# Kernel optimization log

Measured on AMD Instinct MI355X. Metric: run time of the kernel, lower is better.

Reference implementation:

```python
import jax, jax.numpy as jnp
import numpy as np

N = 100000
E = 1000000
HID = 64


def gcn_conv(x, W, b, edge_index, edge_w, num_nodes):
    # PyG GCNConv with edge_weight: add self-loops (weight 1), symmetric norm,
    # out[c] = sum_e norm_e * (x @ W)[row_e] aggregated at col_e, plus bias.
    xw = x @ W  # [N, hid]
    row = jnp.concatenate([edge_index[0], jnp.arange(num_nodes)])
    col = jnp.concatenate([edge_index[1], jnp.arange(num_nodes)])
    ew = jnp.concatenate([edge_w, jnp.ones((num_nodes,), x.dtype)])
    deg = jax.ops.segment_sum(ew, col, num_segments=num_nodes)
    dinv = jnp.where(deg > 0, jax.lax.rsqrt(deg), 0.0)
    norm = dinv[row] * ew * dinv[col]  # [E+N]
    msgs = norm[:, None] * xw[row]  # [E+N, hid]
    out = jax.ops.segment_sum(msgs, col, num_segments=num_nodes)
    return out + b


def setup_inputs() -> dict:
    key = jax.random.key(0)
    ks = jax.random.split(key, 12)
    user_x = jax.random.normal(ks[0], (N, 3), jnp.float32)
    movie_x = jax.random.normal(ks[1], (N, 18), jnp.float32)
    edge_index = jax.random.randint(ks[2], (2, E), 0, N, jnp.int64)
    edge_attr = jax.random.uniform(ks[3], (E,), jnp.float32)
    def lin(k, fan_in, fan_out):
        bound = 1.0 / np.sqrt(fan_in)
        k1, k2 = jax.random.split(k)
        W = jax.random.uniform(k1, (fan_in, fan_out), jnp.float32, -bound, bound)
        b = jax.random.uniform(k2, (fan_out,), jnp.float32, -bound, bound)
        return W, b
    W_user, b_user = lin(ks[4], 3, HID)
    W_movie, b_movie = lin(ks[5], 18, HID)
    W1, b1 = lin(ks[6], 2 * HID, 128)
    W2, b2 = lin(ks[7], 128, 1)
    return {"user_x": user_x, "movie_x": movie_x, "edge_index": edge_index,
            "edge_attr": edge_attr, "W_user": W_user, "b_user": b_user,
            "W_movie": W_movie, "b_movie": b_movie, "W1": W1, "b1": b1,
            "W2": W2, "b2": b2}


def reference(user_x, movie_x, edge_index, edge_attr, W_user, b_user,
              W_movie, b_movie, W1, b1, W2, b2):
    user_out = gcn_conv(user_x, W_user, b_user, edge_index, edge_attr, N)
    movie_out = gcn_conv(movie_x, W_movie, b_movie, edge_index, edge_attr, N)
    h = jnp.concatenate([user_out, movie_out], axis=-1)  # [N, 128]
    h = jax.nn.relu(h @ W1 + b1)
    rating_pred = h @ W2 + b2  # [N, 1]
    return rating_pred
```

## Files before the change

### kernel.cpp

```cpp
#include <hip/hip_runtime.h>
#include <hip/hip_fp16.h>

#define NN 100000
#define NE 1000000
#define BSH 7
#define BCOLS 128
#define NBUCK 782
#define SBLK 256
#define SITER 16
#define CAP 2048
#define OVCAP 16384

__device__ __forceinline__ float2 h2f(unsigned u) {
    union { unsigned u; __half2 h; } c; c.u = u;
    return __half22float2(c.h);
}
__device__ __forceinline__ unsigned f2h2(float a, float b) {
    union { __half2 h; unsigned u; } c; c.h = __floats2half2_rn(a, b);
    return c.u;
}

#define ACC_ROW16(base)                                                      \
    {                                                                        \
        const uint4* pr_ = (const uint4*)(base);                             \
        const uint4 A_ = pr_[0];                                             \
        const uint4 B_ = pr_[1];                                             \
        const uint4 C_ = pr_[2];                                             \
        float2 f_;                                                           \
        f_ = h2f(A_.x); s21[0]  = fmaf(w, f_.x, s21[0]);  s21[1]  = fmaf(w, f_.y, s21[1]);  \
        f_ = h2f(A_.y); s21[2]  = fmaf(w, f_.x, s21[2]);  s21[3]  = fmaf(w, f_.y, s21[3]);  \
        f_ = h2f(A_.z); s21[4]  = fmaf(w, f_.x, s21[4]);  s21[5]  = fmaf(w, f_.y, s21[5]);  \
        f_ = h2f(A_.w); s21[6]  = fmaf(w, f_.x, s21[6]);  s21[7]  = fmaf(w, f_.y, s21[7]);  \
        f_ = h2f(B_.x); s21[8]  = fmaf(w, f_.x, s21[8]);  s21[9]  = fmaf(w, f_.y, s21[9]);  \
        f_ = h2f(B_.y); s21[10] = fmaf(w, f_.x, s21[10]); s21[11] = fmaf(w, f_.y, s21[11]); \
        f_ = h2f(B_.z); s21[12] = fmaf(w, f_.x, s21[12]); s21[13] = fmaf(w, f_.y, s21[13]); \
        f_ = h2f(B_.w); s21[14] = fmaf(w, f_.x, s21[14]); s21[15] = fmaf(w, f_.y, s21[15]); \
        f_ = h2f(C_.x); s21[16] = fmaf(w, f_.x, s21[16]); s21[17] = fmaf(w, f_.y, s21[17]); \
        f_ = h2f(C_.y); s21[18] = fmaf(w, f_.x, s21[18]); s21[19] = fmaf(w, f_.y, s21[19]); \
        f_ = h2f(C_.z); s21[20] = fmaf(w, f_.x, s21[20]);                    \
    }

__global__ __launch_bounds__(128) void fuse_kernel(const float* __restrict__ Wu,
                                                   const float* __restrict__ bu,
                                                   const float* __restrict__ Wm,
                                                   const float* __restrict__ bm,
                                                   const float* __restrict__ W1,
                                                   const float* __restrict__ b1,
                                                   const float* __restrict__ W2,
                                                   float* __restrict__ Mt,
                                                   int* __restrict__ gcur,
                                                   int* __restrict__ ovfn) {
    const int j = threadIdx.x;
    for (int i = j; i < NBUCK; i += 128) gcur[i] = 0;
    if (j == 0) *ovfn = 0;

    float w1c[128];
#pragma unroll
    for (int k = 0; k < 128; k++) w1c[k] = W1[k * 128 + j];

    float* row = Mt + j * 24;
#pragma unroll
    for (int m = 0; m < 3; m++) {
        float acc = 0.f;
#pragma unroll
        for (int k = 0; k < 64; k++) acc = fmaf(Wu[m * 64 + k], w1c[k], acc);
        row[m] = acc;
    }
#pragma unroll
    for (int m = 0; m < 18; m++) {
        float acc = 0.f;
#pragma unroll
        for (int k = 0; k < 64; k++) acc = fmaf(Wm[m * 64 + k], w1c[64 + k], acc);
        row[3 + m] = acc;
    }
    float bp = b1[j];
#pragma unroll
    for (int k = 0; k < 64; k++) {
        bp = fmaf(bu[k], w1c[k], bp);
        bp = fmaf(bm[k], w1c[64 + k], bp);
    }
    row[21] = bp;
    row[22] = W2[j];
    row[23] = 0.f;
}

__global__ __launch_bounds__(256) void bscatter_kernel(const int* __restrict__ ei,
                                                       const float* __restrict__ ew,
                                                       int* __restrict__ gcur,
                                                       int2* __restrict__ mid,
                                                       int4* __restrict__ ovf,
                                                       int* __restrict__ ovfn) {
    __shared__ int h[NBUCK];
    __shared__ int rbase[NBUCK];
    int cs[SITER], rs[SITER];
    float wv[SITER];
    const int e0 = blockIdx.x * 256 + threadIdx.x;

    for (int i = threadIdx.x; i < NBUCK; i += 256) h[i] = 0;
    __syncthreads();
#pragma unroll
    for (int k = 0; k < SITER; k++) {
        const int e = e0 + k * (SBLK * 256);
        if (e < NE) {
            cs[k] = ei[NE + e];
            rs[k] = ei[e];
            wv[k] = ew[e];
            atomicAdd(&h[cs[k] >> BSH], 1);
        }
    }
    __syncthreads();
    for (int i = threadIdx.x; i < NBUCK; i += 256) {
        const int c0 = h[i];
        rbase[i] = c0 ? atomicAdd(&gcur[i], c0) : 0;
        h[i] = 0;
    }
    __syncthreads();
#pragma unroll
    for (int k = 0; k < SITER; k++) {
        const int e = e0 + k * (SBLK * 256);
        if (e < NE) {
            const int bb = cs[k] >> BSH;
            const int pos = rbase[bb] + atomicAdd(&h[bb], 1);
            if (pos < CAP) {
                mid[(size_t)bb * CAP + pos] =
                    make_int2((cs[k] & (BCOLS - 1)) | (rs[k] << BSH),
                              __float_as_int(wv[k]));
            } else {
                const int oi = atomicAdd(ovfn, 1);
                if (oi < OVCAP)
                    ovf[oi] = make_int4(cs[k], rs[k], __float_as_int(wv[k]), 0);
            }
        }
    }
}

__global__ __launch_bounds__(256) void bdeg_pack_kernel(const int2* __restrict__ mid,
                                                        const int* __restrict__ gcur,
                                                        const int* __restrict__ ovfn,
                                                        const int4* __restrict__ ovf,
                                                        const float* __restrict__ ux,
                                                        const float* __restrict__ mx,
                                                        unsigned short* __restrict__ pack16,
                                                        float* __restrict__ dinv) {
    __shared__ float dl[BCOLS];
    const int b = blockIdx.x;
    const int t = threadIdx.x;
    if (t < BCOLS) dl[t] = 0.f;
    __syncthreads();
    const int cntt = gcur[b];
    const int segc = cntt < CAP ? cntt : CAP;
    const int start = b * CAP;
    for (int i = t; i < segc; i += 256) {
        const int2 p = mid[start + i];
        atomicAdd(&dl[p.x & (BCOLS - 1)], __int_as_float(p.y));
    }
    if (cntt > CAP) {
        const int n = min(*ovfn, OVCAP);
        for (int i = t; i < n; i += 256) {
            const int4 q = ovf[i];
            if ((q.x >> BSH) == b)
                atomicAdd(&dl[q.x & (BCOLS - 1)], __int_as_float(q.z));
        }
    }
    __syncthreads();
    if (t < BCOLS) {
        const int r = b * BCOLS + t;
        if (r < NN) {
            const float d = rsqrtf(dl[t] + 1.0f);
            dinv[r] = d;
            float v[22];
            const float* u = ux + (size_t)r * 3;
            const float* m = mx + (size_t)r * 18;
            v[0] = d * u[0];
            v[1] = d * u[1];
            v[2] = d * u[2];
#pragma unroll
            for (int k = 0; k < 18; k++) v[3 + k] = d * m[k];
            v[21] = d;
            unsigned wb[16];
#pragma unroll
            for (int k = 0; k < 11; k++) wb[k] = f2h2(v[2 * k], v[2 * k + 1]);
#pragma unroll
            for (int k = 11; k < 16; k++) wb[k] = 0u;
            uint4* dst = (uint4*)(pack16 + (size_t)r * 32);
            dst[0] = make_uint4(wb[0], wb[1], wb[2], wb[3]);
            dst[1] = make_uint4(wb[4], wb[5], wb[6], wb[7]);
            dst[2] = make_uint4(wb[8], wb[9], wb[10], wb[11]);
            dst[3] = make_uint4(wb[12], wb[13], wb[14], wb[15]);
        }
    }
}

__global__ __launch_bounds__(512) void bagg_mlp_kernel(const int2* __restrict__ mid,
                                                       const int* __restrict__ gcur,
                                                       const int* __restrict__ ovfn,
                                                       const int4* __restrict__ ovf,
                                                       const unsigned short* __restrict__ pack16,
                                                       const float* __restrict__ dinv,
                                                       const float* __restrict__ Mt,
                                                       const float* __restrict__ b2,
                                                       float* __restrict__ out) {
    __shared__ int2 smid[CAP];
    __shared__ int ccnt[BCOLS];
    __shared__ int cbase[BCOLS];
    __shared__ int cptr[BCOLS];
    __shared__ float sfin[BCOLS][33];
    __shared__ float po[3][BCOLS];

    const int b = blockIdx.x;
    const int t = threadIdx.x;
    const int start = b * CAP;
    const int cntt = gcur[b];
    const int segc = cntt < CAP ? cntt : CAP;

    if (t < BCOLS) ccnt[t] = 0;
    __syncthreads();
    for (int i = t; i < segc; i += 512)
        atomicAdd(&ccnt[mid[start + i].x & (BCOLS - 1)], 1);
    __syncthreads();

    if (t < 64) {
        const int a = ccnt[2 * t];
        const int bb = ccnt[2 * t + 1];
        int p = a + bb;
#pragma unroll
        for (int d = 1; d < 64; d <<= 1) {
            const int x = __shfl_up(p, d, 64);
            if (t >= d) p += x;
        }
        cbase[2 * t] = p - bb;
        cbase[2 * t + 1] = p;
        cptr[2 * t] = p - bb - a;
        cptr[2 * t + 1] = p - bb;
    }
    __syncthreads();

    for (int i = t; i < segc; i += 512) {
        const int2 p = mid[start + i];
        const int pos = atomicAdd(&cptr[p.x & (BCOLS - 1)], 1);
        smid[pos] = p;
    }
    __syncthreads();

    {
        const int colq = t >> 2;
        const int slice = t & 3;
        float sacc[8];
#pragma unroll
        for (int m = 0; m < 8; m++) sacc[m] = 0.f;

        const int q0 = (colq == 0) ? 0 : cbase[colq - 1];
        const int q1 = cbase[colq];
        const unsigned short* pbase = pack16 + slice * 8;
#pragma unroll 4
        for (int i = q0; i < q1; i++) {
            const int2 p = smid[i];
            const unsigned row = ((unsigned)p.x) >> BSH;
            const float w = __int_as_float(p.y);
            const uint4 Q = *(const uint4*)(pbase + (size_t)row * 32);
            float2 f;
            f = h2f(Q.x); sacc[0] = fmaf(w, f.x, sacc[0]); sacc[1] = fmaf(w, f.y, sacc[1]);
            f = h2f(Q.y); sacc[2] = fmaf(w, f.x, sacc[2]); sacc[3] = fmaf(w, f.y, sacc[3]);
            f = h2f(Q.z); sacc[4] = fmaf(w, f.x, sacc[4]); sacc[5] = fmaf(w, f.y, sacc[5]);
            f = h2f(Q.w); sacc[6] = fmaf(w, f.x, sacc[6]); sacc[7] = fmaf(w, f.y, sacc[7]);
        }
        if (slice < 3) {
#pragma unroll
            for (int m = 0; m < 8; m++) sfin[colq][slice * 8 + m] = sacc[m];
        }
    }
    __syncthreads();

    {
        const int colq = t >> 2;
        const int slice = t & 3;
        const int cc = b * BCOLS + colq;
        if (slice == 0 && cc < NN) {
            float s21[21];
#pragma unroll
            for (int m = 0; m < 21; m++) s21[m] = sfin[colq][m];
            if (cntt > CAP) {
                const int n = min(*ovfn, OVCAP);
                for (int i = 0; i < n; i++) {
                    const int4 q = ovf[i];
                    if (q.x == cc) {
                        const unsigned row = (unsigned)q.y;
                        const float w = __int_as_float(q.z);
                        ACC_ROW16(pack16 + (size_t)row * 32);
                    }
                }
            }
            {
                const float w = 1.0f;
                ACC_ROW16(pack16 + (size_t)cc * 32);
            }
            const float d = dinv[cc];
#pragma unroll
            for (int m = 0; m < 21; m++) sfin[colq][m] = s21[m] * d;
        }
    }
    __syncthreads();

    const int col = t & (BCOLS - 1);
    const int hf = t >> 7;
    const int c = b * BCOLS + col;
    float s21[21];
#pragma unroll
    for (int m = 0; m < 21; m++) s21[m] = sfin[col][m];
    float o = 0.f;
    if (c < NN) {
        const int k0 = hf * 32;
#pragma unroll 2
        for (int k = k0; k < k0 + 32; k++) {
            const float* r = Mt + k * 24;
            float hsum = r[21];
#pragma unroll
            for (int m = 0; m < 21; m++) hsum = fmaf(s21[m], r[m], hsum);
            o = fmaf(fmaxf(hsum, 0.f), r[22], o);
        }
    }
    if (hf) po[hf - 1][col] = o;
    __syncthreads();
    if (hf == 0 && c < NN)
        out[c] = o + po[0][col] + po[1][col] + po[2][col] + b2[0];
}

extern "C" void kernel_launch(void* const* d_in, const int* in_sizes, int n_in,
                              void* d_out, int out_size, void* d_ws, size_t ws_size,
                              hipStream_t stream) {
    const float* ux = (const float*)d_in[0];
    const float* mx = (const float*)d_in[1];
    const int* ei = (const int*)d_in[2];
    const float* ew = (const float*)d_in[3];
    const float* Wu = (const float*)d_in[4];
    const float* bu = (const float*)d_in[5];
    const float* Wm = (const float*)d_in[6];
    const float* bm = (const float*)d_in[7];
    const float* W1 = (const float*)d_in[8];
    const float* b1 = (const float*)d_in[9];
    const float* W2 = (const float*)d_in[10];
    const float* b2 = (const float*)d_in[11];
    float* out = (float*)d_out;

    char* ws = (char*)d_ws;
    int*            gcur   = (int*)ws;
    int*            ovfn   = (int*)(ws + 4096);
    float*          Mt     = (float*)(ws + 8192);
    float*          dinv   = (float*)(ws + 20480);
    unsigned short* pack16 = (unsigned short*)(ws + 420480);
    int2*           mid    = (int2*)(ws + 6820480);
    int4*           ovf    = (int4*)(ws + 19632768);

    fuse_kernel<<<1, 128, 0, stream>>>(Wu, bu, Wm, bm, W1, b1, W2, Mt, gcur, ovfn);
    bscatter_kernel<<<SBLK, 256, 0, stream>>>(ei, ew, gcur, mid, ovf, ovfn);
    bdeg_pack_kernel<<<NBUCK, 256, 0, stream>>>(mid, gcur, ovfn, ovf, ux, mx, pack16, dinv);
    bagg_mlp_kernel<<<NBUCK, 512, 0, stream>>>(mid, gcur, ovfn, ovf, pack16, dinv, Mt, b2, out);
}
```

Before: 182.0 us.

## Compute degrees with global float atomics in scatter, drop bucket re-read pass

Degree accumulation moves into the scatter kernel as global unsafeAtomicAdd on a new per-node degree array, which the widened init kernel now zeroes. The old degree-and-pack kernel, which re-read the bucketed edge list and scanned the overflow list per bucket, becomes a plain per-node pack kernel. This avoids a second pass over the edge buffer, at the cost of a million global float atomics to scattered addresses and an extra zeroing pass.

```diff
diff --git a/kernel.cpp b/kernel.cpp
--- a/kernel.cpp
+++ b/kernel.cpp
@@ -10,6 +10,7 @@
 #define SITER 16
 #define CAP 2048
 #define OVCAP 16384
+#define ZBLK 320
 
 __device__ __forceinline__ float2 h2f(unsigned u) {
     union { unsigned u; __half2 h; } c; c.u = u;
@@ -40,19 +41,27 @@
         f_ = h2f(C_.z); s21[20] = fmaf(w, f_.x, s21[20]);                    \
     }
 
-__global__ __launch_bounds__(128) void fuse_kernel(const float* __restrict__ Wu,
-                                                   const float* __restrict__ bu,
-                                                   const float* __restrict__ Wm,
-                                                   const float* __restrict__ bm,
-                                                   const float* __restrict__ W1,
-                                                   const float* __restrict__ b1,
-                                                   const float* __restrict__ W2,
-                                                   float* __restrict__ Mt,
-                                                   int* __restrict__ gcur,
-                                                   int* __restrict__ ovfn) {
+__global__ __launch_bounds__(256) void fuse_zero_kernel(const float* __restrict__ Wu,
+                                                        const float* __restrict__ bu,
+                                                        const float* __restrict__ Wm,
+                                                        const float* __restrict__ bm,
+                                                        const float* __restrict__ W1,
+                                                        const float* __restrict__ b1,
+                                                        const float* __restrict__ W2,
+                                                        float* __restrict__ Mt,
+                                                        int* __restrict__ gcur,
+                                                        int* __restrict__ ovfn,
+                                                        float* __restrict__ degf) {
+    if (blockIdx.x != 0) {
+        const int tid = (blockIdx.x - 1) * 256 + threadIdx.x;
+        const int NT = (ZBLK - 1) * 256;
+        for (int i = tid; i < NN; i += NT) degf[i] = 0.f;
+        for (int i = tid; i < NBUCK; i += NT) gcur[i] = 0;
+        if (tid == 0) *ovfn = 0;
+        return;
+    }
     const int j = threadIdx.x;
-    for (int i = j; i < NBUCK; i += 128) gcur[i] = 0;
-    if (j == 0) *ovfn = 0;
+    if (j >= 128) return;
 
     float w1c[128];
 #pragma unroll
@@ -87,6 +96,7 @@
 __global__ __launch_bounds__(256) void bscatter_kernel(const int* __restrict__ ei,
                                                        const float* __restrict__ ew,
                                                        int* __restrict__ gcur,
+                                                       float* __restrict__ degf,
                                                        int2* __restrict__ mid,
                                                        int4* __restrict__ ovf,
                                                        int* __restrict__ ovfn) {
@@ -106,6 +116,7 @@
             rs[k] = ei[e];
             wv[k] = ew[e];
             atomicAdd(&h[cs[k] >> BSH], 1);
+            unsafeAtomicAdd(&degf[cs[k]], wv[k]);
         }
     }
     __syncthreads();
@@ -134,61 +145,34 @@
     }
 }
 
-__global__ __launch_bounds__(256) void bdeg_pack_kernel(const int2* __restrict__ mid,
-                                                        const int* __restrict__ gcur,
-                                                        const int* __restrict__ ovfn,
-                                                        const int4* __restrict__ ovf,
-                                                        const float* __restrict__ ux,
-                                                        const float* __restrict__ mx,
-                                                        unsigned short* __restrict__ pack16,
-                                                        float* __restrict__ dinv) {
-    __shared__ float dl[BCOLS];
-    const int b = blockIdx.x;
-    const int t = threadIdx.x;
-    if (t < BCOLS) dl[t] = 0.f;
-    __syncthreads();
-    const int cntt = gcur[b];
-    const int segc = cntt < CAP ? cntt : CAP;
-    const int start = b * CAP;
-    for (int i = t; i < segc; i += 256) {
-        const int2 p = mid[start + i];
-        atomicAdd(&dl[p.x & (BCOLS - 1)], __int_as_float(p.y));
-    }
-    if (cntt > CAP) {
-        const int n = min(*ovfn, OVCAP);
-        for (int i = t; i < n; i += 256) {
-            const int4 q = ovf[i];
-            if ((q.x >> BSH) == b)
-                atomicAdd(&dl[q.x & (BCOLS - 1)], __int_as_float(q.z));
-        }
-    }
-    __syncthreads();
-    if (t < BCOLS) {
-        const int r = b * BCOLS + t;
-        if (r < NN) {
-            const float d = rsqrtf(dl[t] + 1.0f);
-            dinv[r] = d;
-            float v[22];
-            const float* u = ux + (size_t)r * 3;
-            const float* m = mx + (size_t)r * 18;
-            v[0] = d * u[0];
-            v[1] = d * u[1];
-            v[2] = d * u[2];
-#pragma unroll
-            for (int k = 0; k < 18; k++) v[3 + k] = d * m[k];
-            v[21] = d;
-            unsigned wb[16];
-#pragma unroll
-            for (int k = 0; k < 11; k++) wb[k] = f2h2(v[2 * k], v[2 * k + 1]);
-#pragma unroll
-            for (int k = 11; k < 16; k++) wb[k] = 0u;
-            uint4* dst = (uint4*)(pack16 + (size_t)r * 32);
-            dst[0] = make_uint4(wb[0], wb[1], wb[2], wb[3]);
-            dst[1] = make_uint4(wb[4], wb[5], wb[6], wb[7]);
-            dst[2] = make_uint4(wb[8], wb[9], wb[10], wb[11]);
-            dst[3] = make_uint4(wb[12], wb[13], wb[14], wb[15]);
-        }
-    }
+__global__ __launch_bounds__(256) void pack_kernel(const float* __restrict__ degf,
+                                                   const float* __restrict__ ux,
+                                                   const float* __restrict__ mx,
+                                                   unsigned short* __restrict__ pack16,
+                                                   float* __restrict__ dinv) {
+    const int r = blockIdx.x * 256 + threadIdx.x;
+    if (r >= NN) return;
+    const float d = rsqrtf(degf[r] + 1.0f);
+    dinv[r] = d;
+    float v[22];
+    const float* u = ux + (size_t)r * 3;
+    const float* m = mx + (size_t)r * 18;
+    v[0] = d * u[0];
+    v[1] = d * u[1];
+    v[2] = d * u[2];
+#pragma unroll
+    for (int k = 0; k < 18; k++) v[3 + k] = d * m[k];
+    v[21] = d;
+    unsigned wb[16];
+#pragma unroll
+    for (int k = 0; k < 11; k++) wb[k] = f2h2(v[2 * k], v[2 * k + 1]);
+#pragma unroll
+    for (int k = 11; k < 16; k++) wb[k] = 0u;
+    uint4* dst = (uint4*)(pack16 + (size_t)r * 32);
+    dst[0] = make_uint4(wb[0], wb[1], wb[2], wb[3]);
+    dst[1] = make_uint4(wb[4], wb[5], wb[6], wb[7]);
+    dst[2] = make_uint4(wb[8], wb[9], wb[10], wb[11]);
+    dst[3] = make_uint4(wb[12], wb[13], wb[14], wb[15]);
 }
 
 __global__ __launch_bounds__(512) void bagg_mlp_kernel(const int2* __restrict__ mid,
@@ -347,12 +331,14 @@
     int*            ovfn   = (int*)(ws + 4096);
     float*          Mt     = (float*)(ws + 8192);
     float*          dinv   = (float*)(ws + 20480);
-    unsigned short* pack16 = (unsigned short*)(ws + 420480);
-    int2*           mid    = (int2*)(ws + 6820480);
-    int4*           ovf    = (int4*)(ws + 19632768);
-
-    fuse_kernel<<<1, 128, 0, stream>>>(Wu, bu, Wm, bm, W1, b1, W2, Mt, gcur, ovfn);
-    bscatter_kernel<<<SBLK, 256, 0, stream>>>(ei, ew, gcur, mid, ovf, ovfn);
-    bdeg_pack_kernel<<<NBUCK, 256, 0, stream>>>(mid, gcur, ovfn, ovf, ux, mx, pack16, dinv);
+    float*          degf   = (float*)(ws + 420480);
+    unsigned short* pack16 = (unsigned short*)(ws + 820480);
+    int2*           mid    = (int2*)(ws + 7220480);
+    int4*           ovf    = (int4*)(ws + 20032768);
+
+    fuse_zero_kernel<<<ZBLK, 256, 0, stream>>>(Wu, bu, Wm, bm, W1, b1, W2,
+                                               Mt, gcur, ovfn, degf);
+    bscatter_kernel<<<SBLK, 256, 0, stream>>>(ei, ew, gcur, degf, mid, ovf, ovfn);
+    pack_kernel<<<(NN + 255) / 256, 256, 0, stream>>>(degf, ux, mx, pack16, dinv);
     bagg_mlp_kernel<<<NBUCK, 512, 0, stream>>>(mid, gcur, ovfn, ovf, pack16, dinv, Mt, b2, out);
 }
```

Result: slower. 224.9 us (+23.6%).
